# Kernel optimization log

Hardware: AMD Instinct MI355X
Metric: run time of the kernel (lower is better)

Reference implementation:

```python
import jax, jax.numpy as jnp
import numpy as np

N = 50000
E = 800000
F = 128
H = 128
D = 3

def setup_inputs() -> dict:
    key = jax.random.key(0)
    ks = jax.random.split(key, 12)
    s = lambda fan_in: 1.0 / np.sqrt(fan_in)
    return {
        "node": jax.random.normal(ks[0], (N, F), jnp.float32),
        "coordinate": jax.random.normal(ks[1], (N, D), jnp.float32),
        "edge_index": jax.random.randint(ks[2], (2, E), 0, N, jnp.int32),
        "We1": jax.random.normal(ks[3], (2 * F + 1, H), jnp.float32) * s(2 * F + 1),
        "be1": jnp.zeros((H,), jnp.float32),
        "We2": jax.random.normal(ks[4], (H, H), jnp.float32) * s(H),
        "be2": jnp.zeros((H,), jnp.float32),
        "Wx": jax.random.normal(ks[5], (H, 1), jnp.float32) * s(H),
        "bx": jnp.zeros((1,), jnp.float32),
        "Wh1": jax.random.normal(ks[6], (F + H, H), jnp.float32) * s(F + H),
        "bh1": jnp.zeros((H,), jnp.float32),
        "Wh2": jax.random.normal(ks[7], (H, F), jnp.float32) * s(H),
        "bh2": jnp.zeros((F,), jnp.float32),
    }

def reference(node, coordinate, edge_index, We1, be1, We2, be2, Wx, bx, Wh1, bh1, Wh2, bh2):
    src = edge_index[0]
    dst = edge_index[1]
    n = node.shape[0]
    # gather endpoint features / coords
    h_j = node[src]            # [E, F]
    h_i = node[dst]            # [E, F]
    dist = coordinate[dst] - coordinate[src]          # [E, D] = x_i - x_j
    sqdist = jnp.sum(dist * dist, axis=1, keepdims=True)  # [E, 1]
    # phi_e: Linear -> ReLU -> Linear
    e_in = jnp.concatenate([h_i, h_j, sqdist], axis=-1)    # [E, 2F+1]
    m_ij = jax.nn.relu(e_in @ We1 + be1) @ We2 + be2       # [E, H]
    # phi_x: Linear to scalar edge weight
    w_ij = m_ij @ Wx + bx                                  # [E, 1]
    vec = dist * w_ij                                      # [E, D]
    C = 1.0 / (n - 1)
    delta_x = jax.ops.segment_sum(vec, dst, num_segments=n) * C
    x_new = coordinate + delta_x
    # aggregate messages per target node (sum)
    m_i = jax.ops.segment_sum(m_ij, dst, num_segments=n)   # [N, H]
    # phi_h: Linear -> ReLU -> Linear
    h_in = jnp.concatenate([node, m_i], axis=1)            # [N, F+H]
    h_new = jax.nn.relu(h_in @ Wh1 + bh1) @ Wh2 + bh2      # [N, F]
    return (h_new, x_new)
```

## Files before the change

kernel.cpp:

```cpp
#include <hip/hip_runtime.h>
#include <stdint.h>

#define NN 50000
#define NE 800000
#define NBINS 50001
#define H_OUT_OFF 6400000

typedef float  f32x4  __attribute__((ext_vector_type(4)));
typedef short  bf16x8 __attribute__((ext_vector_type(8)));

static __device__ __forceinline__ unsigned short f2b(float f) {
  unsigned u = __float_as_uint(f);
  return (unsigned short)((u + 0x7fffu + ((u >> 16) & 1u)) >> 16);
}
static __device__ __forceinline__ float b2f(unsigned short h) {
  return __uint_as_float(((unsigned)h) << 16);
}

__global__ void prep_weights_kernel(const float* __restrict__ We1,
                                    const float* __restrict__ We2,
                                    const float* __restrict__ Wh1,
                                    const float* __restrict__ Wh2,
                                    unsigned short* __restrict__ We1Ttop,
                                    unsigned short* __restrict__ We1Tbot,
                                    unsigned short* __restrict__ We2T,
                                    unsigned short* __restrict__ Wh1T,
                                    unsigned short* __restrict__ Wh2T) {
  int i = blockIdx.x * 256 + threadIdx.x;
  if (i < 16384) {
    int n = i >> 7, k = i & 127;
    We1Ttop[i] = f2b(We1[k * 128 + n]);
  } else if (i < 32768) {
    int j = i - 16384; int n = j >> 7, k = j & 127;
    We1Tbot[j] = f2b(We1[(128 + k) * 128 + n]);
  } else if (i < 49152) {
    int j = i - 32768; int n = j >> 7, k = j & 127;
    We2T[j] = f2b(We2[k * 128 + n]);
  } else if (i < 81920) {
    int j = i - 49152; int n = j >> 8, k = j & 255;
    Wh1T[j] = f2b(Wh1[k * 128 + n]);
  } else if (i < 98304) {
    int j = i - 81920; int n = j >> 7, k = j & 127;
    Wh2T[j] = f2b(Wh2[k * 128 + n]);
  }
}

__global__ void uc_kernel(const float* __restrict__ We2, const float* __restrict__ Wx,
                          const float* __restrict__ be2, const float* __restrict__ bx,
                          float* __restrict__ uvec) {
  int k = threadIdx.x;
  if (k < 128) {
    float s = 0.f;
    for (int n = 0; n < 128; n++) s += We2[k * 128 + n] * Wx[n];
    uvec[k] = s;
  } else if (k == 128) {
    float s = 0.f;
    for (int n = 0; n < 128; n++) s += be2[n] * Wx[n];
    uvec[128] = s + bx[0];
  }
}

__global__ void hist_kernel(const int* __restrict__ ei, int* __restrict__ cnt,
                            int* __restrict__ rank) {
  int i = blockIdx.x * 256 + threadIdx.x;
  if (i < NE) rank[i] = atomicAdd(&cnt[ei[NE + i]], 1);
}

__global__ void scanA_kernel(const int* __restrict__ cnt, int* __restrict__ bsum) {
  __shared__ int sd[256];
  int b = blockIdx.x, t = threadIdx.x, i = b * 256 + t;
  sd[t] = (i < NBINS) ? cnt[i] : 0;
  __syncthreads();
  for (int s = 128; s; s >>= 1) {
    if (t < s) sd[t] += sd[t + s];
    __syncthreads();
  }
  if (t == 0) bsum[b] = sd[0];
}

__global__ void scanB_kernel(const int* __restrict__ bsum, int* __restrict__ boffs) {
  __shared__ int sd[256];
  int t = threadIdx.x;
  int v = (t < 196) ? bsum[t] : 0;
  sd[t] = v;
  __syncthreads();
  for (int off = 1; off < 256; off <<= 1) {
    int x = (t >= off) ? sd[t - off] : 0;
    __syncthreads();
    sd[t] += x;
    __syncthreads();
  }
  if (t < 196) boffs[t] = sd[t] - v;
}

__global__ void scanC_kernel(const int* __restrict__ cnt, const int* __restrict__ boffs,
                             int* __restrict__ starts) {
  __shared__ int sd[256];
  int b = blockIdx.x, t = threadIdx.x, i = b * 256 + t;
  int v = (i < NBINS) ? cnt[i] : 0;
  sd[t] = v;
  __syncthreads();
  for (int off = 1; off < 256; off <<= 1) {
    int x = (t >= off) ? sd[t - off] : 0;
    __syncthreads();
    sd[t] += x;
    __syncthreads();
  }
  if (i < NBINS) starts[i] = sd[t] - v + boffs[b];
}

__global__ void scatter_kernel(const int* __restrict__ ei, const int* __restrict__ starts,
                               const int* __restrict__ rank, int* __restrict__ srcs) {
  int i = blockIdx.x * 256 + threadIdx.x;
  if (i < NE) {
    srcs[starts[ei[NE + i]] + rank[i]] = ei[i];
  }
}

__global__ __launch_bounds__(256, 4)
void yz_kernel(const float* __restrict__ node,
               const unsigned short* __restrict__ We1Ttop,
               const unsigned short* __restrict__ We1Tbot,
               const float* __restrict__ be1,
               unsigned short* __restrict__ Yb,
               unsigned short* __restrict__ Zb) {
  __shared__ __align__(16) unsigned short sA[64][136];
  const int tid = threadIdx.x;
  const int n0 = blockIdx.x * 64;

  for (int c = tid; c < 64 * 16; c += 256) {
    int e = c >> 4, s = c & 15;
    int n = n0 + e;
    if (n < NN) {
      const float* p = node + (size_t)n * 128 + s * 8;
      float4 v0 = *(const float4*)p;
      float4 v1 = *(const float4*)(p + 4);
      *(ushort4*)&sA[e][s * 8]     = make_ushort4(f2b(v0.x), f2b(v0.y), f2b(v0.z), f2b(v0.w));
      *(ushort4*)&sA[e][s * 8 + 4] = make_ushort4(f2b(v1.x), f2b(v1.y), f2b(v1.z), f2b(v1.w));
    } else {
      *(uint4*)&sA[e][s * 8] = make_uint4(0, 0, 0, 0);
    }
  }
  __syncthreads();

  const int wave = tid >> 6, lane = tid & 63;
  const int quad = lane >> 4, l16 = lane & 15;
  const int col0 = wave * 32 + l16, col1 = wave * 32 + 16 + l16;

  const f32x4 zero = {0.f, 0.f, 0.f, 0.f};
  f32x4 accY[4][2], accZ[4][2];
#pragma unroll
  for (int mt = 0; mt < 4; mt++) {
    accY[mt][0] = zero; accY[mt][1] = zero;
    accZ[mt][0] = zero; accZ[mt][1] = zero;
  }

#pragma unroll
  for (int kt = 0; kt < 4; kt++) {
    int kb = kt * 32 + quad * 8;
    bf16x8 by0 = *(const bf16x8*)(We1Ttop + (col0 << 7) + kb);
    bf16x8 by1 = *(const bf16x8*)(We1Ttop + (col1 << 7) + kb);
    bf16x8 bz0 = *(const bf16x8*)(We1Tbot + (col0 << 7) + kb);
    bf16x8 bz1 = *(const bf16x8*)(We1Tbot + (col1 << 7) + kb);
#pragma unroll
    for (int mt = 0; mt < 4; mt++) {
      bf16x8 a = *(const bf16x8*)&sA[mt * 16 + l16][kb];
      accY[mt][0] = __builtin_amdgcn_mfma_f32_16x16x32_bf16(a, by0, accY[mt][0], 0, 0, 0);
      accY[mt][1] = __builtin_amdgcn_mfma_f32_16x16x32_bf16(a, by1, accY[mt][1], 0, 0, 0);
      accZ[mt][0] = __builtin_amdgcn_mfma_f32_16x16x32_bf16(a, bz0, accZ[mt][0], 0, 0, 0);
      accZ[mt][1] = __builtin_amdgcn_mfma_f32_16x16x32_bf16(a, bz1, accZ[mt][1], 0, 0, 0);
    }
  }

  float sb0 = be1[col0], sb1 = be1[col1];
#pragma unroll
  for (int mt = 0; mt < 4; mt++) {
#pragma unroll
    for (int r = 0; r < 4; r++) {
      int row = mt * 16 + quad * 4 + r;
      int n = n0 + row;
      if (n < NN) {
        Yb[(size_t)n * 128 + col0] = f2b(accY[mt][0][r] + sb0);
        Yb[(size_t)n * 128 + col1] = f2b(accY[mt][1][r] + sb1);
        Zb[(size_t)n * 128 + col0] = f2b(accZ[mt][0][r]);
        Zb[(size_t)n * 128 + col1] = f2b(accZ[mt][1][r]);
      }
    }
  }
}

__global__ __launch_bounds__(256, 8)
void edge_kernel(const unsigned short* __restrict__ Zb,
                 const unsigned short* __restrict__ Yb,
                 const int* __restrict__ srcs,
                 const int* __restrict__ starts,
                 const float* __restrict__ coord,
                 const float* __restrict__ We1,
                 const float* __restrict__ uvec,
                 float* __restrict__ T,
                 float* __restrict__ out) {
  __shared__ int    sSrc[4][64];
  __shared__ float4 sQ[4][64];
  __shared__ int    sMaxChunks;

  const int tid = threadIdx.x, wave = tid >> 6, lane = tid & 63;
  const int n = blockIdx.x * 4 + wave;
  const int col = lane * 2;

  const int start = starts[n], end = starts[n + 1];
  const int deg = end - start;
  const int chunks = (deg + 63) >> 6;

  if (tid == 0) sMaxChunks = 0;
  __syncthreads();
  if (lane == 0) atomicMax(&sMaxChunks, chunks);
  __syncthreads();
  const int nch = sMaxChunks;

  const float wsq0 = We1[256 * 128 + col], wsq1 = We1[256 * 128 + col + 1];
  const float u0 = uvec[col], u1 = uvec[col + 1];
  const float c  = uvec[128];

  ushort2 yv = *(const ushort2*)&Yb[(size_t)n * 128 + col];
  const float y0 = b2f(yv.x), y1 = b2f(yv.y);
  const float cdx = coord[n * 3 + 0], cdy = coord[n * 3 + 1], cdz = coord[n * 3 + 2];

  float accT0 = 0.f, accT1 = 0.f;
  float sx = 0.f, sy = 0.f, sz = 0.f;
  float dsx = 0.f, dsy = 0.f, dsz = 0.f;

  for (int ch = 0; ch < nch; ch++) {
    int cb = start + ch * 64;
    int m = end - cb; if (m > 64) m = 64;
    if (lane < m) {
      int s = srcs[cb + lane];
      float dx = cdx - coord[s * 3 + 0];
      float dy = cdy - coord[s * 3 + 1];
      float dz = cdz - coord[s * 3 + 2];
      sSrc[wave][lane] = s;
      sQ[wave][lane] = make_float4(dx, dy, dz, dx * dx + dy * dy + dz * dz);
      dsx += dx; dsy += dy; dsz += dz;
    }
    __syncthreads();
#pragma unroll 4
    for (int r = 0; r < m; r++) {
      int ss = sSrc[wave][r];
      float4 q = sQ[wave][r];
      float tmp0 = y0 + q.w * wsq0;
      float tmp1 = y1 + q.w * wsq1;
      ushort2 zv = *(const ushort2*)&Zb[(size_t)ss * 128 + col];
      float t0 = fmaxf(b2f(zv.x) + tmp0, 0.f);
      float t1 = fmaxf(b2f(zv.y) + tmp1, 0.f);
      accT0 += t0; accT1 += t1;
      float tu = t0 * u0 + t1 * u1;
      sx += tu * q.x; sy += tu * q.y; sz += tu * q.z;
    }
    __syncthreads();
  }

  *(float2*)&T[(size_t)n * 128 + col] = make_float2(accT0, accT1);

  float px = sx + c * dsx, py = sy + c * dsy, pz = sz + c * dsz;
#pragma unroll
  for (int o = 1; o < 64; o <<= 1) {
    px += __shfl_xor(px, o); py += __shfl_xor(py, o); pz += __shfl_xor(pz, o);
  }
  if (lane == 0) {
    const float C = 1.0f / 49999.0f;
    out[H_OUT_OFF + n * 3 + 0] = cdx + C * px;
    out[H_OUT_OFF + n * 3 + 1] = cdy + C * py;
    out[H_OUT_OFF + n * 3 + 2] = cdz + C * pz;
  }
}

__global__ __launch_bounds__(256, 3)
void node_kernel(const float* __restrict__ node,
                 const float* __restrict__ T,
                 const int* __restrict__ starts,
                 const unsigned short* __restrict__ We2T,
                 const float* __restrict__ be2,
                 const unsigned short* __restrict__ Wh1T,
                 const float* __restrict__ bh1,
                 const unsigned short* __restrict__ Wh2T,
                 const float* __restrict__ bh2,
                 float* __restrict__ out) {
  __shared__ __align__(16) unsigned short sA[64][264];
  __shared__ __align__(16) unsigned short sT[64][136];
  __shared__ float sDeg[64];

  const int tid = threadIdx.x;
  const int n0 = blockIdx.x * 64;

  if (tid < 64) {
    int n = n0 + tid;
    sDeg[tid] = (n < NN) ? (float)(starts[n + 1] - starts[n]) : 0.f;
  }

  for (int c = tid; c < 64 * 16; c += 256) {
    int e = c >> 4, s = c & 15;
    int n = n0 + e;
    if (n < NN) {
      const float* pn = node + (size_t)n * 128 + s * 8;
      float4 a0 = *(const float4*)pn;
      float4 a1 = *(const float4*)(pn + 4);
      *(ushort4*)&sA[e][s * 8]     = make_ushort4(f2b(a0.x), f2b(a0.y), f2b(a0.z), f2b(a0.w));
      *(ushort4*)&sA[e][s * 8 + 4] = make_ushort4(f2b(a1.x), f2b(a1.y), f2b(a1.z), f2b(a1.w));
      const float* p = T + (size_t)n * 128 + s * 8;
      float4 v0 = *(const float4*)p;
      float4 v1 = *(const float4*)(p + 4);
      *(ushort4*)&sT[e][s * 8]     = make_ushort4(f2b(v0.x), f2b(v0.y), f2b(v0.z), f2b(v0.w));
      *(ushort4*)&sT[e][s * 8 + 4] = make_ushort4(f2b(v1.x), f2b(v1.y), f2b(v1.z), f2b(v1.w));
    } else {
      *(uint4*)&sA[e][s * 8] = make_uint4(0, 0, 0, 0);
      *(uint4*)&sT[e][s * 8] = make_uint4(0, 0, 0, 0);
    }
  }
  __syncthreads();

  const int wave = tid >> 6, lane = tid & 63;
  const int quad = lane >> 4, l16 = lane & 15;
  const int col0 = wave * 32 + l16, col1 = wave * 32 + 16 + l16;

  const f32x4 zero = {0.f, 0.f, 0.f, 0.f};

  f32x4 accM[4][2];
#pragma unroll
  for (int mt = 0; mt < 4; mt++) { accM[mt][0] = zero; accM[mt][1] = zero; }
#pragma unroll
  for (int kt = 0; kt < 4; kt++) {
    int kb = kt * 32 + quad * 8;
    bf16x8 b0 = *(const bf16x8*)(We2T + (col0 << 7) + kb);
    bf16x8 b1 = *(const bf16x8*)(We2T + (col1 << 7) + kb);
#pragma unroll
    for (int mt = 0; mt < 4; mt++) {
      bf16x8 a = *(const bf16x8*)&sT[mt * 16 + l16][kb];
      accM[mt][0] = __builtin_amdgcn_mfma_f32_16x16x32_bf16(a, b0, accM[mt][0], 0, 0, 0);
      accM[mt][1] = __builtin_amdgcn_mfma_f32_16x16x32_bf16(a, b1, accM[mt][1], 0, 0, 0);
    }
  }
  {
    float eb0 = be2[col0], eb1 = be2[col1];
#pragma unroll
    for (int mt = 0; mt < 4; mt++) {
#pragma unroll
      for (int r = 0; r < 4; r++) {
        int row = mt * 16 + quad * 4 + r;
        float dg = sDeg[row];
        sA[row][128 + col0] = f2b(accM[mt][0][r] + dg * eb0);
        sA[row][128 + col1] = f2b(accM[mt][1][r] + dg * eb1);
      }
    }
  }
  __syncthreads();

  f32x4 acc[4][2];
#pragma unroll
  for (int mt = 0; mt < 4; mt++) { acc[mt][0] = zero; acc[mt][1] = zero; }
#pragma unroll
  for (int kt = 0; kt < 8; kt++) {
    int kb = kt * 32 + quad * 8;
    bf16x8 b0 = *(const bf16x8*)(Wh1T + (col0 << 8) + kb);
    bf16x8 b1 = *(const bf16x8*)(Wh1T + (col1 << 8) + kb);
#pragma unroll
    for (int mt = 0; mt < 4; mt++) {
      bf16x8 a = *(const bf16x8*)&sA[mt * 16 + l16][kb];
      acc[mt][0] = __builtin_amdgcn_mfma_f32_16x16x32_bf16(a, b0, acc[mt][0], 0, 0, 0);
      acc[mt][1] = __builtin_amdgcn_mfma_f32_16x16x32_bf16(a, b1, acc[mt][1], 0, 0, 0);
    }
  }
  {
    float sb0 = bh1[col0], sb1 = bh1[col1];
#pragma unroll
    for (int mt = 0; mt < 4; mt++) {
#pragma unroll
      for (int r = 0; r < 4; r++) {
        int row = mt * 16 + quad * 4 + r;
        sT[row][col0] = f2b(fmaxf(acc[mt][0][r] + sb0, 0.f));
        sT[row][col1] = f2b(fmaxf(acc[mt][1][r] + sb1, 0.f));
      }
    }
  }
  __syncthreads();

  f32x4 acc2[4][2];
#pragma unroll
  for (int mt = 0; mt < 4; mt++) { acc2[mt][0] = zero; acc2[mt][1] = zero; }
#pragma unroll
  for (int kt = 0; kt < 4; kt++) {
    int kb = kt * 32 + quad * 8;
    bf16x8 b0 = *(const bf16x8*)(Wh2T + (col0 << 7) + kb);
    bf16x8 b1 = *(const bf16x8*)(Wh2T + (col1 << 7) + kb);
#pragma unroll
    for (int mt = 0; mt < 4; mt++) {
      bf16x8 a = *(const bf16x8*)&sT[mt * 16 + l16][kb];
      acc2[mt][0] = __builtin_amdgcn_mfma_f32_16x16x32_bf16(a, b0, acc2[mt][0], 0, 0, 0);
      acc2[mt][1] = __builtin_amdgcn_mfma_f32_16x16x32_bf16(a, b1, acc2[mt][1], 0, 0, 0);
    }
  }
  {
    float eb0 = bh2[col0], eb1 = bh2[col1];
#pragma unroll
    for (int mt = 0; mt < 4; mt++) {
#pragma unroll
      for (int r = 0; r < 4; r++) {
        int row = mt * 16 + quad * 4 + r;
        int n = n0 + row;
        if (n < NN) {
          out[(size_t)n * 128 + col0] = acc2[mt][0][r] + eb0;
          out[(size_t)n * 128 + col1] = acc2[mt][1][r] + eb1;
        }
      }
    }
  }
}

extern "C" void kernel_launch(void* const* d_in, const int* in_sizes, int n_in,
                              void* d_out, int out_size, void* d_ws, size_t ws_size,
                              hipStream_t stream) {
  const float* node  = (const float*)d_in[0];
  const float* coord = (const float*)d_in[1];
  const int*   ei    = (const int*)d_in[2];
  const float* We1   = (const float*)d_in[3];
  const float* be1   = (const float*)d_in[4];
  const float* We2   = (const float*)d_in[5];
  const float* be2   = (const float*)d_in[6];
  const float* Wx    = (const float*)d_in[7];
  const float* bx    = (const float*)d_in[8];
  const float* Wh1   = (const float*)d_in[9];
  const float* bh1   = (const float*)d_in[10];
  const float* Wh2   = (const float*)d_in[11];
  const float* bh2   = (const float*)d_in[12];
  float* out = (float*)d_out;

  char* ws = (char*)d_ws;
  float* T       = (float*)(ws);
  int*   cnt     = (int*)  (ws + 25600000);
  int*   starts  = (int*)  (ws + 25800704);
  int*   bsum    = (int*)  (ws + 26001408);
  int*   boffs   = (int*)  (ws + 26002432);
  int*   rank    = (int*)  (ws + 26003456);
  int*   srcs    = (int*)  (ws + 29203456);
  unsigned short* Yb      = (unsigned short*)(ws + 32403456);
  unsigned short* Zb      = (unsigned short*)(ws + 45203456);
  unsigned short* We1Ttop = (unsigned short*)(ws + 58003456);
  unsigned short* We1Tbot = (unsigned short*)(ws + 58036224);
  unsigned short* We2T    = (unsigned short*)(ws + 58068992);
  unsigned short* Wh1T    = (unsigned short*)(ws + 58101760);
  unsigned short* Wh2T    = (unsigned short*)(ws + 58167296);
  float* uvec    = (float*)(ws + 58200064);

  hipMemsetAsync(cnt, 0, 200704, stream);

  prep_weights_kernel<<<384, 256, 0, stream>>>(We1, We2, Wh1, Wh2,
                                               We1Ttop, We1Tbot, We2T, Wh1T, Wh2T);
  uc_kernel<<<1, 192, 0, stream>>>(We2, Wx, be2, bx, uvec);
  hist_kernel<<<3125, 256, 0, stream>>>(ei, cnt, rank);
  scanA_kernel<<<196, 256, 0, stream>>>(cnt, bsum);
  scanB_kernel<<<1, 256, 0, stream>>>(bsum, boffs);
  scanC_kernel<<<196, 256, 0, stream>>>(cnt, boffs, starts);
  scatter_kernel<<<3125, 256, 0, stream>>>(ei, starts, rank, srcs);
  yz_kernel<<<(NN + 63) / 64, 256, 0, stream>>>(node, We1Ttop, We1Tbot, be1, Yb, Zb);
  edge_kernel<<<NN / 4, 256, 0, stream>>>(Zb, Yb, srcs, starts, coord, We1, uvec,
                                          T, out);
  node_kernel<<<(NN + 63) / 64, 256, 0, stream>>>(node, T, starts, We2T, be2,
                                                  Wh1T, bh1, Wh2T, bh2, out);
}
```

Before: 274.3 us.

## Merge preprocessing launches, single-block scan, 16-bit CSR indices, dual-edge wave processing

```diff
diff --git a/kernel.cpp b/kernel.cpp
--- a/kernel.cpp
+++ b/kernel.cpp
@@ -17,38 +17,50 @@
   return __uint_as_float(((unsigned)h) << 16);
 }
 
-__global__ void prep_weights_kernel(const float* __restrict__ We1,
-                                    const float* __restrict__ We2,
-                                    const float* __restrict__ Wh1,
-                                    const float* __restrict__ Wh2,
-                                    unsigned short* __restrict__ We1Ttop,
-                                    unsigned short* __restrict__ We1Tbot,
-                                    unsigned short* __restrict__ We2T,
-                                    unsigned short* __restrict__ Wh1T,
-                                    unsigned short* __restrict__ Wh2T) {
-  int i = blockIdx.x * 256 + threadIdx.x;
-  if (i < 16384) {
-    int n = i >> 7, k = i & 127;
-    We1Ttop[i] = f2b(We1[k * 128 + n]);
-  } else if (i < 32768) {
-    int j = i - 16384; int n = j >> 7, k = j & 127;
-    We1Tbot[j] = f2b(We1[(128 + k) * 128 + n]);
-  } else if (i < 49152) {
-    int j = i - 32768; int n = j >> 7, k = j & 127;
-    We2T[j] = f2b(We2[k * 128 + n]);
-  } else if (i < 81920) {
-    int j = i - 49152; int n = j >> 8, k = j & 255;
-    Wh1T[j] = f2b(Wh1[k * 128 + n]);
-  } else if (i < 98304) {
-    int j = i - 81920; int n = j >> 7, k = j & 127;
-    Wh2T[j] = f2b(Wh2[k * 128 + n]);
-  }
-}
-
-__global__ void uc_kernel(const float* __restrict__ We2, const float* __restrict__ Wx,
-                          const float* __restrict__ be2, const float* __restrict__ bx,
+__global__ void k1_kernel(const int* __restrict__ ei,
+                          int* __restrict__ cnt,
+                          unsigned short* __restrict__ rank,
+                          const float* __restrict__ We1,
+                          const float* __restrict__ We2,
+                          const float* __restrict__ Wh1,
+                          const float* __restrict__ Wh2,
+                          const float* __restrict__ be2,
+                          const float* __restrict__ Wx,
+                          const float* __restrict__ bx,
+                          unsigned short* __restrict__ We1Ttop,
+                          unsigned short* __restrict__ We1Tbot,
+                          unsigned short* __restrict__ We2T,
+                          unsigned short* __restrict__ Wh1T,
+                          unsigned short* __restrict__ Wh2T,
                           float* __restrict__ uvec) {
-  int k = threadIdx.x;
+  int b = blockIdx.x, tid = threadIdx.x;
+  if (b < 3125) {
+    int i = b * 256 + tid;
+    if (i < NE) rank[i] = (unsigned short)atomicAdd(&cnt[ei[NE + i]], 1);
+    return;
+  }
+  b -= 3125;
+  if (b < 384) {
+    int i = b * 256 + tid;
+    if (i < 16384) {
+      int n = i >> 7, k = i & 127;
+      We1Ttop[i] = f2b(We1[k * 128 + n]);
+    } else if (i < 32768) {
+      int j = i - 16384; int n = j >> 7, k = j & 127;
+      We1Tbot[j] = f2b(We1[(128 + k) * 128 + n]);
+    } else if (i < 49152) {
+      int j = i - 32768; int n = j >> 7, k = j & 127;
+      We2T[j] = f2b(We2[k * 128 + n]);
+    } else if (i < 81920) {
+      int j = i - 49152; int n = j >> 8, k = j & 255;
+      Wh1T[j] = f2b(Wh1[k * 128 + n]);
+    } else if (i < 98304) {
+      int j = i - 81920; int n = j >> 7, k = j & 127;
+      Wh2T[j] = f2b(Wh2[k * 128 + n]);
+    }
+    return;
+  }
+  int k = tid;
   if (k < 128) {
     float s = 0.f;
     for (int n = 0; n < 128; n++) s += We2[k * 128 + n] * Wx[n];
@@ -60,65 +72,37 @@
   }
 }
 
-__global__ void hist_kernel(const int* __restrict__ ei, int* __restrict__ cnt,
-                            int* __restrict__ rank) {
-  int i = blockIdx.x * 256 + threadIdx.x;
-  if (i < NE) rank[i] = atomicAdd(&cnt[ei[NE + i]], 1);
-}
-
-__global__ void scanA_kernel(const int* __restrict__ cnt, int* __restrict__ bsum) {
-  __shared__ int sd[256];
-  int b = blockIdx.x, t = threadIdx.x, i = b * 256 + t;
-  sd[t] = (i < NBINS) ? cnt[i] : 0;
+__global__ __launch_bounds__(1024)
+void scan_kernel(const int* __restrict__ cnt, int* __restrict__ starts) {
+  __shared__ int sS[1024];
+  const int t = threadIdx.x;
+  const int base = t * 49;
+  int sum = 0;
+  for (int i = 0; i < 49; i++) {
+    int idx = base + i;
+    if (idx < NBINS) sum += cnt[idx];
+  }
+  sS[t] = sum;
   __syncthreads();
-  for (int s = 128; s; s >>= 1) {
-    if (t < s) sd[t] += sd[t + s];
+  for (int off = 1; off < 1024; off <<= 1) {
+    int v = (t >= off) ? sS[t - off] : 0;
     __syncthreads();
-  }
-  if (t == 0) bsum[b] = sd[0];
-}
-
-__global__ void scanB_kernel(const int* __restrict__ bsum, int* __restrict__ boffs) {
-  __shared__ int sd[256];
-  int t = threadIdx.x;
-  int v = (t < 196) ? bsum[t] : 0;
-  sd[t] = v;
-  __syncthreads();
-  for (int off = 1; off < 256; off <<= 1) {
-    int x = (t >= off) ? sd[t - off] : 0;
+    sS[t] += v;
     __syncthreads();
-    sd[t] += x;
-    __syncthreads();
-  }
-  if (t < 196) boffs[t] = sd[t] - v;
-}
-
-__global__ void scanC_kernel(const int* __restrict__ cnt, const int* __restrict__ boffs,
-                             int* __restrict__ starts) {
-  __shared__ int sd[256];
-  int b = blockIdx.x, t = threadIdx.x, i = b * 256 + t;
-  int v = (i < NBINS) ? cnt[i] : 0;
-  sd[t] = v;
-  __syncthreads();
-  for (int off = 1; off < 256; off <<= 1) {
-    int x = (t >= off) ? sd[t - off] : 0;
-    __syncthreads();
-    sd[t] += x;
-    __syncthreads();
-  }
-  if (i < NBINS) starts[i] = sd[t] - v + boffs[b];
-}
-
-__global__ void scatter_kernel(const int* __restrict__ ei, const int* __restrict__ starts,
-                               const int* __restrict__ rank, int* __restrict__ srcs) {
-  int i = blockIdx.x * 256 + threadIdx.x;
-  if (i < NE) {
-    srcs[starts[ei[NE + i]] + rank[i]] = ei[i];
+  }
+  int run = sS[t] - sum;
+  for (int i = 0; i < 49; i++) {
+    int idx = base + i;
+    if (idx < NBINS) { starts[idx] = run; run += cnt[idx]; }
   }
 }
 
 __global__ __launch_bounds__(256, 4)
-void yz_kernel(const float* __restrict__ node,
+void k3_kernel(const int* __restrict__ ei,
+               const unsigned short* __restrict__ rank,
+               const int* __restrict__ starts,
+               unsigned short* __restrict__ srcs,
+               const float* __restrict__ node,
                const unsigned short* __restrict__ We1Ttop,
                const unsigned short* __restrict__ We1Tbot,
                const float* __restrict__ be1,
@@ -126,7 +110,17 @@
                unsigned short* __restrict__ Zb) {
   __shared__ __align__(16) unsigned short sA[64][136];
   const int tid = threadIdx.x;
-  const int n0 = blockIdx.x * 64;
+  int b = blockIdx.x;
+
+  if (b < 3125) {
+    int i = b * 256 + tid;
+    if (i < NE) {
+      srcs[starts[ei[NE + i]] + (int)rank[i]] = (unsigned short)ei[i];
+    }
+    return;
+  }
+  b -= 3125;
+  const int n0 = b * 64;
 
   for (int c = tid; c < 64 * 16; c += 256) {
     int e = c >> 4, s = c & 15;
@@ -192,7 +186,7 @@
 __global__ __launch_bounds__(256, 8)
 void edge_kernel(const unsigned short* __restrict__ Zb,
                  const unsigned short* __restrict__ Yb,
-                 const int* __restrict__ srcs,
+                 const unsigned short* __restrict__ srcs,
                  const int* __restrict__ starts,
                  const float* __restrict__ coord,
                  const float* __restrict__ We1,
@@ -201,64 +195,61 @@
                  float* __restrict__ out) {
   __shared__ int    sSrc[4][64];
   __shared__ float4 sQ[4][64];
-  __shared__ int    sMaxChunks;
 
   const int tid = threadIdx.x, wave = tid >> 6, lane = tid & 63;
   const int n = blockIdx.x * 4 + wave;
-  const int col = lane * 2;
+  const int half = lane >> 5, l32 = lane & 31;
+  const int col = l32 * 4;
 
   const int start = starts[n], end = starts[n + 1];
-  const int deg = end - start;
-  const int chunks = (deg + 63) >> 6;
-
-  if (tid == 0) sMaxChunks = 0;
-  __syncthreads();
-  if (lane == 0) atomicMax(&sMaxChunks, chunks);
-  __syncthreads();
-  const int nch = sMaxChunks;
-
-  const float wsq0 = We1[256 * 128 + col], wsq1 = We1[256 * 128 + col + 1];
-  const float u0 = uvec[col], u1 = uvec[col + 1];
-  const float c  = uvec[128];
-
-  ushort2 yv = *(const ushort2*)&Yb[(size_t)n * 128 + col];
-  const float y0 = b2f(yv.x), y1 = b2f(yv.y);
+
+  const float4 wsq = *(const float4*)(We1 + 256 * 128 + col);
+  const float4 u   = *(const float4*)(uvec + col);
+  const float  c   = uvec[128];
+  ushort4 yv = *(const ushort4*)(Yb + (size_t)n * 128 + col);
+  const float y0 = b2f(yv.x), y1 = b2f(yv.y), y2 = b2f(yv.z), y3 = b2f(yv.w);
   const float cdx = coord[n * 3 + 0], cdy = coord[n * 3 + 1], cdz = coord[n * 3 + 2];
 
-  float accT0 = 0.f, accT1 = 0.f;
+  float aT0 = 0.f, aT1 = 0.f, aT2 = 0.f, aT3 = 0.f;
   float sx = 0.f, sy = 0.f, sz = 0.f;
   float dsx = 0.f, dsy = 0.f, dsz = 0.f;
 
-  for (int ch = 0; ch < nch; ch++) {
-    int cb = start + ch * 64;
+  for (int cb = start; cb < end; cb += 64) {
     int m = end - cb; if (m > 64) m = 64;
+    int s = 0; float dx = 0.f, dy = 0.f, dz = 0.f;
     if (lane < m) {
-      int s = srcs[cb + lane];
-      float dx = cdx - coord[s * 3 + 0];
-      float dy = cdy - coord[s * 3 + 1];
-      float dz = cdz - coord[s * 3 + 2];
-      sSrc[wave][lane] = s;
-      sQ[wave][lane] = make_float4(dx, dy, dz, dx * dx + dy * dy + dz * dz);
+      s = (int)srcs[cb + lane];
+      dx = cdx - coord[s * 3 + 0];
+      dy = cdy - coord[s * 3 + 1];
+      dz = cdz - coord[s * 3 + 2];
       dsx += dx; dsy += dy; dsz += dz;
     }
-    __syncthreads();
-#pragma unroll 4
-    for (int r = 0; r < m; r++) {
-      int ss = sSrc[wave][r];
-      float4 q = sQ[wave][r];
-      float tmp0 = y0 + q.w * wsq0;
-      float tmp1 = y1 + q.w * wsq1;
-      ushort2 zv = *(const ushort2*)&Zb[(size_t)ss * 128 + col];
-      float t0 = fmaxf(b2f(zv.x) + tmp0, 0.f);
-      float t1 = fmaxf(b2f(zv.y) + tmp1, 0.f);
-      accT0 += t0; accT1 += t1;
-      float tu = t0 * u0 + t1 * u1;
+    sSrc[wave][lane] = s;
+    sQ[wave][lane] = make_float4(dx, dy, dz, dx * dx + dy * dy + dz * dz);
+    __builtin_amdgcn_wave_barrier();
+    int pairs = (m + 1) >> 1;
+    for (int p = 0; p < pairs; p++) {
+      int idx = 2 * p + half;
+      int ss = sSrc[wave][idx];
+      float4 q = sQ[wave][idx];
+      float valid = (idx < m) ? 1.f : 0.f;
+      ushort4 zv = *(const ushort4*)(Zb + (size_t)ss * 128 + col);
+      float t0 = fmaxf(b2f(zv.x) + y0 + q.w * wsq.x, 0.f) * valid;
+      float t1 = fmaxf(b2f(zv.y) + y1 + q.w * wsq.y, 0.f) * valid;
+      float t2 = fmaxf(b2f(zv.z) + y2 + q.w * wsq.z, 0.f) * valid;
+      float t3 = fmaxf(b2f(zv.w) + y3 + q.w * wsq.w, 0.f) * valid;
+      aT0 += t0; aT1 += t1; aT2 += t2; aT3 += t3;
+      float tu = t0 * u.x + t1 * u.y + t2 * u.z + t3 * u.w;
       sx += tu * q.x; sy += tu * q.y; sz += tu * q.z;
     }
-    __syncthreads();
-  }
-
-  *(float2*)&T[(size_t)n * 128 + col] = make_float2(accT0, accT1);
+    __builtin_amdgcn_wave_barrier();
+  }
+
+  aT0 += __shfl_xor(aT0, 32); aT1 += __shfl_xor(aT1, 32);
+  aT2 += __shfl_xor(aT2, 32); aT3 += __shfl_xor(aT3, 32);
+  if (half == 0) {
+    *(float4*)&T[(size_t)n * 128 + col] = make_float4(aT0, aT1, aT2, aT3);
+  }
 
   float px = sx + c * dsx, py = sy + c * dsy, pz = sz + c * dsz;
 #pragma unroll
@@ -433,35 +424,30 @@
   float* out = (float*)d_out;
 
   char* ws = (char*)d_ws;
-  float* T       = (float*)(ws);
-  int*   cnt     = (int*)  (ws + 25600000);
-  int*   starts  = (int*)  (ws + 25800704);
-  int*   bsum    = (int*)  (ws + 26001408);
-  int*   boffs   = (int*)  (ws + 26002432);
-  int*   rank    = (int*)  (ws + 26003456);
-  int*   srcs    = (int*)  (ws + 29203456);
-  unsigned short* Yb      = (unsigned short*)(ws + 32403456);
-  unsigned short* Zb      = (unsigned short*)(ws + 45203456);
-  unsigned short* We1Ttop = (unsigned short*)(ws + 58003456);
-  unsigned short* We1Tbot = (unsigned short*)(ws + 58036224);
-  unsigned short* We2T    = (unsigned short*)(ws + 58068992);
-  unsigned short* Wh1T    = (unsigned short*)(ws + 58101760);
-  unsigned short* Wh2T    = (unsigned short*)(ws + 58167296);
-  float* uvec    = (float*)(ws + 58200064);
+  float*          T      = (float*)(ws);
+  int*            cnt    = (int*)  (ws + 25600000);
+  int*            starts = (int*)  (ws + 25800704);
+  unsigned short* rank   = (unsigned short*)(ws + 26001408);
+  unsigned short* srcs   = (unsigned short*)(ws + 27601408);
+  unsigned short* Yb     = (unsigned short*)(ws + 29201408);
+  unsigned short* Zb     = (unsigned short*)(ws + 42001408);
+  unsigned short* We1Ttop= (unsigned short*)(ws + 54801408);
+  unsigned short* We1Tbot= (unsigned short*)(ws + 54834176);
+  unsigned short* We2T   = (unsigned short*)(ws + 54866944);
+  unsigned short* Wh1T   = (unsigned short*)(ws + 54899712);
+  unsigned short* Wh2T   = (unsigned short*)(ws + 54965248);
+  float*          uvec   = (float*)(ws + 54998016);
 
   hipMemsetAsync(cnt, 0, 200704, stream);
 
-  prep_weights_kernel<<<384, 256, 0, stream>>>(We1, We2, Wh1, Wh2,
-                                               We1Ttop, We1Tbot, We2T, Wh1T, Wh2T);
-  uc_kernel<<<1, 192, 0, stream>>>(We2, Wx, be2, bx, uvec);
-  hist_kernel<<<3125, 256, 0, stream>>>(ei, cnt, rank);
-  scanA_kernel<<<196, 256, 0, stream>>>(cnt, bsum);
-  scanB_kernel<<<1, 256, 0, stream>>>(bsum, boffs);
-  scanC_kernel<<<196, 256, 0, stream>>>(cnt, boffs, starts);
-  scatter_kernel<<<3125, 256, 0, stream>>>(ei, starts, rank, srcs);
-  yz_kernel<<<(NN + 63) / 64, 256, 0, stream>>>(node, We1Ttop, We1Tbot, be1, Yb, Zb);
+  k1_kernel<<<3510, 256, 0, stream>>>(ei, cnt, rank, We1, We2, Wh1, Wh2,
+                                      be2, Wx, bx,
+                                      We1Ttop, We1Tbot, We2T, Wh1T, Wh2T, uvec);
+  scan_kernel<<<1, 1024, 0, stream>>>(cnt, starts);
+  k3_kernel<<<3907, 256, 0, stream>>>(ei, rank, starts, srcs,
+                                      node, We1Ttop, We1Tbot, be1, Yb, Zb);
   edge_kernel<<<NN / 4, 256, 0, stream>>>(Zb, Yb, srcs, starts, coord, We1, uvec,
                                           T, out);
-  node_kernel<<<(NN + 63) / 64, 256, 0, stream>>>(node, T, starts, We2T, be2,
-                                                  Wh1T, bh1, Wh2T, bh2, out);
-}
+  node_kernel<<<782, 256, 0, stream>>>(node, T, starts, We2T, be2,
+                                       Wh1T, bh1, Wh2T, bh2, out);
+}
```

After: 330.4 us. 20.5% more time.
